# Kernel optimization log

Hardware: AMD Instinct MI355X
Metric: run time of the kernel (lower is better)

Reference implementation:

```python
import jax, jax.numpy as jnp
import numpy as np

D_MODEL = 2048
NUM_HEADS = 16
HEAD_DIM = D_MODEL // NUM_HEADS
B, T = 2, 2048


def setup_inputs() -> dict:
    key = jax.random.key(0)
    ks = jax.random.split(key, 6)
    x = jax.random.normal(ks[0], (B, T, D_MODEL), dtype=jnp.float32)
    # RoPE tables: angles theta_i = 10000^(-2i/d), half-dim tables [T, HEAD_DIM//2]
    pos = jnp.arange(T, dtype=jnp.float32)[:, None]
    inv_freq = 1.0 / (10000.0 ** (jnp.arange(0, HEAD_DIM, 2, dtype=jnp.float32) / HEAD_DIM))
    ang = pos * inv_freq[None, :]
    sin = jnp.sin(ang)
    cos = jnp.cos(ang)
    doc_ids = jnp.sort(jax.random.randint(ks[1], (B, T), 0, 4), axis=-1).astype(jnp.int32)
    W_qkv = jax.random.normal(ks[2], (D_MODEL, D_MODEL + 2 * HEAD_DIM), dtype=jnp.float32) * 0.02
    W_out = jax.random.normal(ks[3], (D_MODEL, D_MODEL), dtype=jnp.float32) * 0.02
    return {"x": x, "sin": sin, "cos": cos, "doc_ids": doc_ids, "W_qkv": W_qkv, "W_out": W_out}


def _apply_rope(x, sin, cos):
    # x: [..., T, ..., HEAD_DIM]; sin/cos: [T, HEAD_DIM//2], broadcast to x's rank
    if x.ndim == 4:  # [B, T, H, D]
        s, c = sin[None, :, None, :], cos[None, :, None, :]
    else:  # [B, T, D]
        s, c = sin[None, :, :], cos[None, :, :]
    x1, x2 = jnp.split(x, 2, axis=-1)
    return jnp.concatenate([x1 * c - x2 * s, x2 * c + x1 * s], axis=-1)


def reference(x, sin, cos, doc_ids, W_qkv, W_out):
    b, t, _ = x.shape
    qkv = x @ W_qkv  # [B, T, D_MODEL + 2*HEAD_DIM]
    q = qkv[..., :D_MODEL].reshape(b, t, NUM_HEADS, HEAD_DIM)
    k = qkv[..., D_MODEL:D_MODEL + HEAD_DIM]  # [B, T, HEAD_DIM] single KV head
    v = qkv[..., D_MODEL + HEAD_DIM:]         # [B, T, HEAD_DIM]
    q = _apply_rope(q, sin, cos)
    k = _apply_rope(k, sin, cos)
    # doc-packed causal mask -> additive bias [B, 1, T, T]
    neg_inf = jnp.finfo(q.dtype).min / 2
    causal = jnp.tril(jnp.ones((t, t), dtype=jnp.bool_))
    same_doc = doc_ids[:, :, None] == doc_ids[:, None, :]
    mask = (causal[None, :, :] & same_doc)[:, None, :, :]
    bias = jnp.where(mask, jnp.array(0.0, q.dtype), neg_inf)
    scale = 1.0 / jnp.sqrt(jnp.array(HEAD_DIM, q.dtype))
    scores = jnp.einsum("bthd,bsd->bhts", q, k) * scale + bias  # [B, H, T, T]
    attn = jax.nn.softmax(scores, axis=-1)
    out = jnp.einsum("bhts,bsd->bthd", attn, v).reshape(b, t, D_MODEL)
    return out @ W_out
```

## Files before the change

kernel.cpp:

```cpp
#include <hip/hip_runtime.h>
#include <math.h>

#define D_MODEL 2048
#define NUM_HEADS 16
#define HEAD_DIM 128
#define BB 2
#define TT 2048
#define QKV_N 2304
#define KOFF 2048
#define VOFF 2176

typedef __attribute__((ext_vector_type(8))) short short8;
typedef __attribute__((ext_vector_type(4))) float f32x4;

static __device__ __forceinline__ short f2bf(float f) {
  union { float f; unsigned u; } x; x.f = f;
  unsigned r = (x.u + 0x7FFFu + ((x.u >> 16) & 1u)) >> 16;
  return (short)r;
}
static __device__ __forceinline__ float bf2f(unsigned short u) {
  return __uint_as_float(((unsigned)u) << 16);
}

#define GLD16(gp, lp)                                              \
  __builtin_amdgcn_global_load_lds(                                \
      (const __attribute__((address_space(1))) void*)(gp),         \
      (__attribute__((address_space(3))) void*)(lp), 16, 0, 0)

static __device__ __forceinline__ void swizzle_xy(int& bx, int& by) {
  const int gx = gridDim.x;
  const int lin = blockIdx.y * gx + blockIdx.x;
  const int band = lin / (gx * 8);
  const int rem = lin - band * gx * 8;
  by = band * 8 + (rem & 7);
  bx = rem >> 3;
}

__global__ __launch_bounds__(256) void gemm_qkv_rope(
    const short* __restrict__ A, const short* __restrict__ Bt,
    short* __restrict__ qkv, short* __restrict__ Vtb,
    const float* __restrict__ sin_t, const float* __restrict__ cos_t)
{
  __shared__ short As[2 * 128 * 32];
  __shared__ short Bs[2 * 128 * 32];
  const int K = D_MODEL;

  int bx, by;
  swizzle_xy(bx, by);

  const int tid = threadIdx.x;
  const int w = tid >> 6, l = tid & 63;
  const int quad = l >> 4, l16 = l & 15;
  const int wm = w >> 1, wn = w & 1;
  const int m0 = by * 128, n0 = bx * 128;

  f32x4 acc[4][4];
#pragma unroll
  for (int i = 0; i < 4; i++)
#pragma unroll
    for (int j = 0; j < 4; j++) acc[i][j] = (f32x4){0.f, 0.f, 0.f, 0.f};

  const short* aA = A + (size_t)(m0 + w * 32 + (l >> 2)) * K + (l & 3) * 8;
  const short* aB = Bt + (size_t)(n0 + w * 32 + (l >> 2)) * K + (l & 3) * 8;
  short* lA0 = As + (w * 2) * 512;
  short* lA1 = As + (w * 2 + 1) * 512;
  short* lB0 = Bs + (w * 2) * 512;
  short* lB1 = Bs + (w * 2 + 1) * 512;

  const short* Ard = As + (size_t)(wm * 64 + l16) * 32 + quad * 8;
  const short* Brd = Bs + (size_t)(wn * 16 + l16) * 32 + quad * 8;

  for (int k0 = 0; k0 < K; k0 += 64) {
    __syncthreads();
#pragma unroll
    for (int h = 0; h < 2; h++) {
      const int go = k0 + h * 32;
      const int lo = h * 4096;
      GLD16(aA + go, lA0 + lo);
      GLD16(aA + go + (size_t)16 * K, lA1 + lo);
      GLD16(aB + go, lB0 + lo);
      GLD16(aB + go + (size_t)16 * K, lB1 + lo);
    }
    __syncthreads();

#pragma unroll
    for (int kc = 0; kc < 2; kc++) {
      short8 af[4], bf[4];
#pragma unroll
      for (int mi = 0; mi < 4; mi++)
        af[mi] = *(const short8*)(Ard + kc * 4096 + mi * 512);
#pragma unroll
      for (int ni = 0; ni < 4; ni++)
        bf[ni] = *(const short8*)(Brd + kc * 4096 + ni * 1024);
#pragma unroll
      for (int mi = 0; mi < 4; mi++)
#pragma unroll
        for (int ni = 0; ni < 4; ni++)
          acc[mi][ni] =
              __builtin_amdgcn_mfma_f32_16x16x32_bf16(af[mi], bf[ni], acc[mi][ni], 0, 0, 0);
    }
  }

  const int colbase = wn * 16 + l16;
  const bool is_v = (n0 == VOFF);

#pragma unroll
  for (int mi = 0; mi < 4; mi++) {
#pragma unroll
    for (int r = 0; r < 4; r++) {
      const int row = m0 + wm * 64 + mi * 16 + quad * 4 + r;
      const int b = row >> 11, t = row & (TT - 1);
#pragma unroll
      for (int ni = 0; ni < 2; ni++) {
        const int cloc = ni * 32 + colbase;
        const float c1 = acc[mi][ni][r];
        const float c2 = acc[mi][ni + 2][r];
        if (!is_v) {
          const float sn = sin_t[t * 64 + cloc];
          const float cs = cos_t[t * 64 + cloc];
          short* op = qkv + (size_t)row * QKV_N + n0 + cloc;
          op[0]  = f2bf(c1 * cs - c2 * sn);
          op[64] = f2bf(c2 * cs + c1 * sn);
        } else {
          Vtb[((size_t)(b * 128 + cloc) << 11) + t]      = f2bf(c1);
          Vtb[((size_t)(b * 128 + cloc + 64) << 11) + t] = f2bf(c2);
        }
      }
    }
  }
}

__global__ __launch_bounds__(256) void gemm_mfma_bt(
    const short* __restrict__ A, const short* __restrict__ Bt,
    float* __restrict__ C, int M, int N, int K)
{
  __shared__ short As[2 * 128 * 32];
  __shared__ short Bs[2 * 128 * 32];

  int bx, by;
  swizzle_xy(bx, by);

  const int tid = threadIdx.x;
  const int w = tid >> 6, l = tid & 63;
  const int quad = l >> 4, l16 = l & 15;
  const int wm = w >> 1, wn = w & 1;
  const int m0 = by * 128, n0 = bx * 128;

  f32x4 acc[4][4];
#pragma unroll
  for (int i = 0; i < 4; i++)
#pragma unroll
    for (int j = 0; j < 4; j++) acc[i][j] = (f32x4){0.f, 0.f, 0.f, 0.f};

  const short* aA = A + (size_t)(m0 + w * 32 + (l >> 2)) * K + (l & 3) * 8;
  const short* aB = Bt + (size_t)(n0 + w * 32 + (l >> 2)) * K + (l & 3) * 8;
  short* lA0 = As + (w * 2) * 512;
  short* lA1 = As + (w * 2 + 1) * 512;
  short* lB0 = Bs + (w * 2) * 512;
  short* lB1 = Bs + (w * 2 + 1) * 512;

  const short* Ard = As + (size_t)(wm * 64 + l16) * 32 + quad * 8;
  const short* Brd = Bs + (size_t)(wn * 64 + l16) * 32 + quad * 8;

  for (int k0 = 0; k0 < K; k0 += 64) {
    __syncthreads();
#pragma unroll
    for (int h = 0; h < 2; h++) {
      const int go = k0 + h * 32;
      const int lo = h * 4096;
      GLD16(aA + go, lA0 + lo);
      GLD16(aA + go + (size_t)16 * K, lA1 + lo);
      GLD16(aB + go, lB0 + lo);
      GLD16(aB + go + (size_t)16 * K, lB1 + lo);
    }
    __syncthreads();

#pragma unroll
    for (int kc = 0; kc < 2; kc++) {
      short8 af[4], bf[4];
#pragma unroll
      for (int mi = 0; mi < 4; mi++)
        af[mi] = *(const short8*)(Ard + kc * 4096 + mi * 512);
#pragma unroll
      for (int ni = 0; ni < 4; ni++)
        bf[ni] = *(const short8*)(Brd + kc * 4096 + ni * 512);
#pragma unroll
      for (int mi = 0; mi < 4; mi++)
#pragma unroll
        for (int ni = 0; ni < 4; ni++)
          acc[mi][ni] =
              __builtin_amdgcn_mfma_f32_16x16x32_bf16(af[mi], bf[ni], acc[mi][ni], 0, 0, 0);
    }
  }

#pragma unroll
  for (int mi = 0; mi < 4; mi++) {
#pragma unroll
    for (int ni = 0; ni < 4; ni++) {
#pragma unroll
      for (int r = 0; r < 4; r++) {
        const int row = m0 + wm * 64 + mi * 16 + quad * 4 + r;
        const int col = n0 + wn * 64 + ni * 16 + l16;
        C[(size_t)row * N + col] = acc[mi][ni][r];
      }
    }
  }
}

#define XB_BLOCKS 8192
#define WQ_BLOCKS (72 * 64)
#define WO_BLOCKS (64 * 64)

__global__ __launch_bounds__(256) void prep_all(
    const float* __restrict__ x, short* __restrict__ xb,
    const float* __restrict__ Wq, short* __restrict__ Wqt,
    const float* __restrict__ Wo, short* __restrict__ Wot)
{
  const int bid = blockIdx.x;
  const int tid = threadIdx.x;

  if (bid < XB_BLOCKS) {
    const size_t i4 = (size_t)bid * 256 + tid;
    float4 v = *(const float4*)(x + i4 * 4);
    short4 o;
    o.x = f2bf(v.x); o.y = f2bf(v.y); o.z = f2bf(v.z); o.w = f2bf(v.w);
    *(short4*)(xb + i4 * 4) = o;
    return;
  }

  __shared__ float t[32][33];
  const float* W;
  short* Wt;
  int N, tile, ntx;
  if (bid < XB_BLOCKS + WQ_BLOCKS) {
    tile = bid - XB_BLOCKS; W = Wq; Wt = Wqt; N = QKV_N; ntx = 72;
  } else {
    tile = bid - XB_BLOCKS - WQ_BLOCKS; W = Wo; Wt = Wot; N = D_MODEL; ntx = 64;
  }
  const int K = D_MODEL;
  const int bx = tile % ntx, byy = tile / ntx;
  const int tx = tid & 31, ty = tid >> 5;
  const int n0 = bx * 32, k0 = byy * 32;
#pragma unroll
  for (int j = 0; j < 4; j++)
    t[ty + j * 8][tx] = W[(size_t)(k0 + ty + j * 8) * N + n0 + tx];
  __syncthreads();
#pragma unroll
  for (int j = 0; j < 4; j++)
    Wt[(size_t)(n0 + ty + j * 8) * K + k0 + tx] = f2bf(t[tx][ty + j * 8]);
}

#define KSTR 136
#define VSTR 72
#define PSTR 72

__global__ __launch_bounds__(256) void attn_mfma(
    const short* __restrict__ qkv, const short* __restrict__ Vtb,
    const int* __restrict__ doc_ids, short* __restrict__ attn_out)
{
  __shared__ short Ks[64 * KSTR];
  __shared__ short Vt[128 * VSTR];
  __shared__ short Pbuf[4 * 16 * PSTR];
  __shared__ int doc_s[64];

  const int qt = blockIdx.x, h = blockIdx.y, b = blockIdx.z;
  const int q0 = qt * 64;
  const int tid = threadIdx.x;
  const int w = tid >> 6;
  const int lane = tid & 63;
  const int quad = lane >> 4, l16 = lane & 15;

  const short* qp = qkv + (size_t)(b * TT + q0 + w * 16 + l16) * QKV_N
                    + h * HEAD_DIM + quad * 8;
  short8 Qf[4];
#pragma unroll
  for (int kc = 0; kc < 4; kc++) Qf[kc] = *(const short8*)(qp + kc * 32);

  const int docmin_q = doc_ids[b * TT + q0];
  const int docmax_q = doc_ids[b * TT + q0 + 63];

  int qg[4], mydoc[4];
  float l_i[4];
#pragma unroll
  for (int r = 0; r < 4; r++) {
    qg[r] = q0 + w * 16 + quad * 4 + r;
    mydoc[r] = doc_ids[b * TT + qg[r]];
    l_i[r] = 0.f;
  }
  f32x4 O[8];
#pragma unroll
  for (int v8 = 0; v8 < 8; v8++) O[v8] = (f32x4){0.f, 0.f, 0.f, 0.f};

  short* Pw = Pbuf + w * 16 * PSTR;
  const float scale = 0.08838834764831844f;

  for (int st = 0; st <= qt; st++) {
    const int s0 = st * 64;
    const int dmin_s = doc_ids[b * TT + s0];
    const int dmax_s = doc_ids[b * TT + s0 + 63];
    if (dmax_s < docmin_q) continue;
    const bool full = (st < qt) && (dmin_s == docmax_q);

    __syncthreads();
#pragma unroll
    for (int i = 0; i < 4; i++) {
      int f = i * 256 + tid;
      int row = f >> 4, seg = f & 15;
      int4 v = *(const int4*)(qkv + (size_t)(b * TT + s0 + row) * QKV_N + KOFF + seg * 8);
      *(int4*)(Ks + row * KSTR + seg * 8) = v;
    }
#pragma unroll
    for (int i = 0; i < 4; i++) {
      int f = i * 256 + tid;
      int n = f >> 3, seg = f & 7;
      int4 v = *(const int4*)(Vtb + ((size_t)(b * 128 + n) << 11) + s0 + seg * 8);
      *(int4*)(Vt + n * VSTR + seg * 8) = v;
    }
    if (!full && tid < 64) doc_s[tid] = doc_ids[b * TT + s0 + tid];
    __syncthreads();

    f32x4 S[4];
#pragma unroll
    for (int ns = 0; ns < 4; ns++) {
      f32x4 acc = (f32x4){0.f, 0.f, 0.f, 0.f};
      const short* kr = Ks + (ns * 16 + l16) * KSTR + quad * 8;
#pragma unroll
      for (int kc = 0; kc < 4; kc++) {
        short8 kf = *(const short8*)(kr + kc * 32);
        acc = __builtin_amdgcn_mfma_f32_16x16x32_bf16(Qf[kc], kf, acc, 0, 0, 0);
      }
      S[ns] = acc;
    }

    if (full) {
#pragma unroll
      for (int ns = 0; ns < 4; ns++)
#pragma unroll
        for (int r = 0; r < 4; r++) {
          const float p = __expf(S[ns][r] * scale);
          l_i[r] += p;
          Pw[(quad * 4 + r) * PSTR + ns * 16 + l16] = f2bf(p);
        }
    } else {
#pragma unroll
      for (int ns = 0; ns < 4; ns++) {
        const int s_loc = ns * 16 + l16;
        const int sg = s0 + s_loc;
        const int sdoc = doc_s[s_loc];
#pragma unroll
        for (int r = 0; r < 4; r++) {
          const bool ok = (sg <= qg[r]) && (sdoc == mydoc[r]);
          const float p = ok ? __expf(S[ns][r] * scale) : 0.f;
          l_i[r] += p;
          Pw[(quad * 4 + r) * PSTR + ns * 16 + l16] = f2bf(p);
        }
      }
    }

#pragma unroll
    for (int ks = 0; ks < 2; ks++) {
      short8 pf = *(const short8*)(Pw + l16 * PSTR + ks * 32 + quad * 8);
#pragma unroll
      for (int v8 = 0; v8 < 8; v8++) {
        short8 vf = *(const short8*)(Vt + (v8 * 16 + l16) * VSTR + ks * 32 + quad * 8);
        O[v8] = __builtin_amdgcn_mfma_f32_16x16x32_bf16(pf, vf, O[v8], 0, 0, 0);
      }
    }
  }

#pragma unroll
  for (int off = 8; off >= 1; off >>= 1)
#pragma unroll
    for (int r = 0; r < 4; r++) l_i[r] += __shfl_xor(l_i[r], off);

#pragma unroll
  for (int r = 0; r < 4; r++) {
    const float inv = 1.f / l_i[r];
    short* op = attn_out + (size_t)(b * TT + qg[r]) * D_MODEL + h * HEAD_DIM + l16;
#pragma unroll
    for (int v8 = 0; v8 < 8; v8++)
      op[v8 * 16] = f2bf(O[v8][r] * inv);
  }
}

extern "C" void kernel_launch(void* const* d_in, const int* in_sizes, int n_in,
                              void* d_out, int out_size, void* d_ws, size_t ws_size,
                              hipStream_t stream)
{
  const float* x     = (const float*)d_in[0];
  const float* sin_t = (const float*)d_in[1];
  const float* cos_t = (const float*)d_in[2];
  const int*   doc   = (const int*)  d_in[3];
  const float* W_qkv = (const float*)d_in[4];
  const float* W_out = (const float*)d_in[5];
  float* out = (float*)d_out;

  const int M = BB * TT;

  char* p = (char*)d_ws;
  short* qkv_bf = (short*)p; p += (size_t)M * QKV_N * 2;
  short* xb     = (short*)p; p += (size_t)M * D_MODEL * 2;
  short* attn_bf = xb;
  short* Vtb    = (short*)p; p += (size_t)BB * 128 * TT * 2;
  short* Wqkv_t = (short*)p; p += (size_t)QKV_N * D_MODEL * 2;
  short* Wout_t = (short*)p;

  prep_all<<<XB_BLOCKS + WQ_BLOCKS + WO_BLOCKS, 256, 0, stream>>>(
      x, xb, W_qkv, Wqkv_t, W_out, Wout_t);

  {
    dim3 grid(QKV_N / 128, M / 128);
    gemm_qkv_rope<<<grid, 256, 0, stream>>>(xb, Wqkv_t, qkv_bf, Vtb, sin_t, cos_t);
  }
  {
    dim3 grid(TT / 64, NUM_HEADS, BB);
    attn_mfma<<<grid, 256, 0, stream>>>(qkv_bf, Vtb, doc, attn_bf);
  }
  {
    dim3 grid(D_MODEL / 128, M / 128);
    gemm_mfma_bt<<<grid, 256, 0, stream>>>(attn_bf, Wout_t, out, M, D_MODEL, D_MODEL);
  }
}
```

Baseline: 271.7 us.

## Double-buffer LDS tiles and XOR-swizzle layout in both GEMM kernels

Both GEMM kernels now use two LDS buffers, so the next K-tile is loaded with global_load_lds while MFMAs run on the current tile, and one barrier per iteration is removed. The LDS column chunks are XOR-swizzled on the global-load side and unswizzled on read, to cut LDS bank conflicts on the short8 fragment reads. This doubles LDS use per block, which may lower occupancy. Correctness depends on the swizzle being consistent between the async-load addresses and the fragment reads.

```diff
diff --git a/kernel.cpp b/kernel.cpp
--- a/kernel.cpp
+++ b/kernel.cpp
@@ -41,8 +41,8 @@
     short* __restrict__ qkv, short* __restrict__ Vtb,
     const float* __restrict__ sin_t, const float* __restrict__ cos_t)
 {
-  __shared__ short As[2 * 128 * 32];
-  __shared__ short Bs[2 * 128 * 32];
+  __shared__ short As[2][2 * 128 * 32];
+  __shared__ short Bs[2][2 * 128 * 32];
   const int K = D_MODEL;
 
   int bx, by;
@@ -60,38 +60,40 @@
 #pragma unroll
     for (int j = 0; j < 4; j++) acc[i][j] = (f32x4){0.f, 0.f, 0.f, 0.f};
 
-  const short* aA = A + (size_t)(m0 + w * 32 + (l >> 2)) * K + (l & 3) * 8;
-  const short* aB = Bt + (size_t)(n0 + w * 32 + (l >> 2)) * K + (l & 3) * 8;
-  short* lA0 = As + (w * 2) * 512;
-  short* lA1 = As + (w * 2 + 1) * 512;
-  short* lB0 = Bs + (w * 2) * 512;
-  short* lB1 = Bs + (w * 2 + 1) * 512;
-
-  const short* Ard = As + (size_t)(wm * 64 + l16) * 32 + quad * 8;
-  const short* Brd = Bs + (size_t)(wn * 16 + l16) * 32 + quad * 8;
-
-  for (int k0 = 0; k0 < K; k0 += 64) {
-    __syncthreads();
+  const int cswz = ((l & 3) ^ ((l >> 3) & 3)) * 8;
+  const short* aA = A + (size_t)(m0 + w * 32 + (l >> 2)) * K + cswz;
+  const short* aB = Bt + (size_t)(n0 + w * 32 + (l >> 2)) * K + cswz;
+  const int lwo = w * 1024;
+
+  const int aswz = (quad ^ ((l16 >> 1) & 3)) * 8;
+  const short* Ard = &As[0][0] + (size_t)(wm * 64 + l16) * 32 + aswz;
+  const short* Brd = &Bs[0][0] + (size_t)(wn * 16 + l16) * 32 + aswz;
+
+  auto stage = [&](int buf, int go0) {
 #pragma unroll
     for (int h = 0; h < 2; h++) {
-      const int go = k0 + h * 32;
-      const int lo = h * 4096;
-      GLD16(aA + go, lA0 + lo);
-      GLD16(aA + go + (size_t)16 * K, lA1 + lo);
-      GLD16(aB + go, lB0 + lo);
-      GLD16(aB + go + (size_t)16 * K, lB1 + lo);
-    }
-    __syncthreads();
-
+      const int go = go0 + h * 32;
+      short* la = &As[buf][0] + h * 4096 + lwo;
+      short* lb = &Bs[buf][0] + h * 4096 + lwo;
+      GLD16(aA + go, la);
+      GLD16(aA + go + (size_t)16 * K, la + 512);
+      GLD16(aB + go, lb);
+      GLD16(aB + go + (size_t)16 * K, lb + 512);
+    }
+  };
+
+  auto compute = [&](int buf) {
+    const short* Ac = Ard + buf * 8192;
+    const short* Bc = Brd + buf * 8192;
 #pragma unroll
     for (int kc = 0; kc < 2; kc++) {
       short8 af[4], bf[4];
 #pragma unroll
       for (int mi = 0; mi < 4; mi++)
-        af[mi] = *(const short8*)(Ard + kc * 4096 + mi * 512);
+        af[mi] = *(const short8*)(Ac + kc * 4096 + mi * 512);
 #pragma unroll
       for (int ni = 0; ni < 4; ni++)
-        bf[ni] = *(const short8*)(Brd + kc * 4096 + ni * 1024);
+        bf[ni] = *(const short8*)(Bc + kc * 4096 + ni * 1024);
 #pragma unroll
       for (int mi = 0; mi < 4; mi++)
 #pragma unroll
@@ -99,7 +101,19 @@
           acc[mi][ni] =
               __builtin_amdgcn_mfma_f32_16x16x32_bf16(af[mi], bf[ni], acc[mi][ni], 0, 0, 0);
     }
-  }
+  };
+
+  stage(0, 0);
+  __syncthreads();
+  int cur = 0;
+#pragma unroll 2
+  for (int k0 = 64; k0 < K; k0 += 64) {
+    stage(cur ^ 1, k0);
+    compute(cur);
+    __syncthreads();
+    cur ^= 1;
+  }
+  compute(cur);
 
   const int colbase = wn * 16 + l16;
   const bool is_v = (n0 == VOFF);
@@ -134,8 +148,8 @@
     const short* __restrict__ A, const short* __restrict__ Bt,
     float* __restrict__ C, int M, int N, int K)
 {
-  __shared__ short As[2 * 128 * 32];
-  __shared__ short Bs[2 * 128 * 32];
+  __shared__ short As[2][2 * 128 * 32];
+  __shared__ short Bs[2][2 * 128 * 32];
 
   int bx, by;
   swizzle_xy(bx, by);
@@ -152,38 +166,40 @@
 #pragma unroll
     for (int j = 0; j < 4; j++) acc[i][j] = (f32x4){0.f, 0.f, 0.f, 0.f};
 
-  const short* aA = A + (size_t)(m0 + w * 32 + (l >> 2)) * K + (l & 3) * 8;
-  const short* aB = Bt + (size_t)(n0 + w * 32 + (l >> 2)) * K + (l & 3) * 8;
-  short* lA0 = As + (w * 2) * 512;
-  short* lA1 = As + (w * 2 + 1) * 512;
-  short* lB0 = Bs + (w * 2) * 512;
-  short* lB1 = Bs + (w * 2 + 1) * 512;
-
-  const short* Ard = As + (size_t)(wm * 64 + l16) * 32 + quad * 8;
-  const short* Brd = Bs + (size_t)(wn * 64 + l16) * 32 + quad * 8;
-
-  for (int k0 = 0; k0 < K; k0 += 64) {
-    __syncthreads();
+  const int cswz = ((l & 3) ^ ((l >> 3) & 3)) * 8;
+  const short* aA = A + (size_t)(m0 + w * 32 + (l >> 2)) * K + cswz;
+  const short* aB = Bt + (size_t)(n0 + w * 32 + (l >> 2)) * K + cswz;
+  const int lwo = w * 1024;
+
+  const int aswz = (quad ^ ((l16 >> 1) & 3)) * 8;
+  const short* Ard = &As[0][0] + (size_t)(wm * 64 + l16) * 32 + aswz;
+  const short* Brd = &Bs[0][0] + (size_t)(wn * 64 + l16) * 32 + aswz;
+
+  auto stage = [&](int buf, int go0) {
 #pragma unroll
     for (int h = 0; h < 2; h++) {
-      const int go = k0 + h * 32;
-      const int lo = h * 4096;
-      GLD16(aA + go, lA0 + lo);
-      GLD16(aA + go + (size_t)16 * K, lA1 + lo);
-      GLD16(aB + go, lB0 + lo);
-      GLD16(aB + go + (size_t)16 * K, lB1 + lo);
-    }
-    __syncthreads();
-
+      const int go = go0 + h * 32;
+      short* la = &As[buf][0] + h * 4096 + lwo;
+      short* lb = &Bs[buf][0] + h * 4096 + lwo;
+      GLD16(aA + go, la);
+      GLD16(aA + go + (size_t)16 * K, la + 512);
+      GLD16(aB + go, lb);
+      GLD16(aB + go + (size_t)16 * K, lb + 512);
+    }
+  };
+
+  auto compute = [&](int buf) {
+    const short* Ac = Ard + buf * 8192;
+    const short* Bc = Brd + buf * 8192;
 #pragma unroll
     for (int kc = 0; kc < 2; kc++) {
       short8 af[4], bf[4];
 #pragma unroll
       for (int mi = 0; mi < 4; mi++)
-        af[mi] = *(const short8*)(Ard + kc * 4096 + mi * 512);
+        af[mi] = *(const short8*)(Ac + kc * 4096 + mi * 512);
 #pragma unroll
       for (int ni = 0; ni < 4; ni++)
-        bf[ni] = *(const short8*)(Brd + kc * 4096 + ni * 512);
+        bf[ni] = *(const short8*)(Bc + kc * 4096 + ni * 512);
 #pragma unroll
       for (int mi = 0; mi < 4; mi++)
 #pragma unroll
@@ -191,7 +207,19 @@
           acc[mi][ni] =
               __builtin_amdgcn_mfma_f32_16x16x32_bf16(af[mi], bf[ni], acc[mi][ni], 0, 0, 0);
     }
-  }
+  };
+
+  stage(0, 0);
+  __syncthreads();
+  int cur = 0;
+#pragma unroll 2
+  for (int k0 = 64; k0 < K; k0 += 64) {
+    stage(cur ^ 1, k0);
+    compute(cur);
+    __syncthreads();
+    cur ^= 1;
+  }
+  compute(cur);
 
 #pragma unroll
   for (int mi = 0; mi < 4; mi++) {
```

Measured after the change: 314.6 us. +15.8%, slower.

## Swizzle GEMM LDS tiles and register-prefetch K/V tiles in attention

Applied to the files above, without the earlier changes.

Both GEMM kernels get an XOR swizzle on the 16-byte column chunk for global-to-LDS loads and the matching MFMA fragment reads, meant to cut LDS bank conflicts. The attention kernel computes the first relevant key tile with a wave ballot instead of skipping tiles one by one. It then prefetches the next K/V tile into registers while the current tile is being computed, overlapping global loads with MFMA work. It also raises wave priority around the MFMA sections with s_setprio. The cost is more register pressure, and correctness relies on the swizzle matching between writes and reads.

```diff
diff --git a/kernel.cpp b/kernel.cpp
--- a/kernel.cpp
+++ b/kernel.cpp
@@ -60,15 +60,15 @@
 #pragma unroll
     for (int j = 0; j < 4; j++) acc[i][j] = (f32x4){0.f, 0.f, 0.f, 0.f};
 
-  const short* aA = A + (size_t)(m0 + w * 32 + (l >> 2)) * K + (l & 3) * 8;
-  const short* aB = Bt + (size_t)(n0 + w * 32 + (l >> 2)) * K + (l & 3) * 8;
-  short* lA0 = As + (w * 2) * 512;
-  short* lA1 = As + (w * 2 + 1) * 512;
-  short* lB0 = Bs + (w * 2) * 512;
-  short* lB1 = Bs + (w * 2 + 1) * 512;
-
-  const short* Ard = As + (size_t)(wm * 64 + l16) * 32 + quad * 8;
-  const short* Brd = Bs + (size_t)(wn * 16 + l16) * 32 + quad * 8;
+  const int cswz = ((l & 3) ^ ((l >> 3) & 3)) * 8;
+  const short* aA = A + (size_t)(m0 + w * 32 + (l >> 2)) * K + cswz;
+  const short* aB = Bt + (size_t)(n0 + w * 32 + (l >> 2)) * K + cswz;
+  short* lA = As + w * 1024;
+  short* lB = Bs + w * 1024;
+
+  const int aswz = (quad ^ ((l16 >> 1) & 3)) * 8;
+  const short* Ard = As + (size_t)(wm * 64 + l16) * 32 + aswz;
+  const short* Brd = Bs + (size_t)(wn * 16 + l16) * 32 + aswz;
 
   for (int k0 = 0; k0 < K; k0 += 64) {
     __syncthreads();
@@ -76,10 +76,10 @@
     for (int h = 0; h < 2; h++) {
       const int go = k0 + h * 32;
       const int lo = h * 4096;
-      GLD16(aA + go, lA0 + lo);
-      GLD16(aA + go + (size_t)16 * K, lA1 + lo);
-      GLD16(aB + go, lB0 + lo);
-      GLD16(aB + go + (size_t)16 * K, lB1 + lo);
+      GLD16(aA + go, lA + lo);
+      GLD16(aA + go + (size_t)16 * K, lA + lo + 512);
+      GLD16(aB + go, lB + lo);
+      GLD16(aB + go + (size_t)16 * K, lB + lo + 512);
     }
     __syncthreads();
 
@@ -152,15 +152,15 @@
 #pragma unroll
     for (int j = 0; j < 4; j++) acc[i][j] = (f32x4){0.f, 0.f, 0.f, 0.f};
 
-  const short* aA = A + (size_t)(m0 + w * 32 + (l >> 2)) * K + (l & 3) * 8;
-  const short* aB = Bt + (size_t)(n0 + w * 32 + (l >> 2)) * K + (l & 3) * 8;
-  short* lA0 = As + (w * 2) * 512;
-  short* lA1 = As + (w * 2 + 1) * 512;
-  short* lB0 = Bs + (w * 2) * 512;
-  short* lB1 = Bs + (w * 2 + 1) * 512;
-
-  const short* Ard = As + (size_t)(wm * 64 + l16) * 32 + quad * 8;
-  const short* Brd = Bs + (size_t)(wn * 64 + l16) * 32 + quad * 8;
+  const int cswz = ((l & 3) ^ ((l >> 3) & 3)) * 8;
+  const short* aA = A + (size_t)(m0 + w * 32 + (l >> 2)) * K + cswz;
+  const short* aB = Bt + (size_t)(n0 + w * 32 + (l >> 2)) * K + cswz;
+  short* lA = As + w * 1024;
+  short* lB = Bs + w * 1024;
+
+  const int aswz = (quad ^ ((l16 >> 1) & 3)) * 8;
+  const short* Ard = As + (size_t)(wm * 64 + l16) * 32 + aswz;
+  const short* Brd = Bs + (size_t)(wn * 64 + l16) * 32 + aswz;
 
   for (int k0 = 0; k0 < K; k0 += 64) {
     __syncthreads();
@@ -168,10 +168,10 @@
     for (int h = 0; h < 2; h++) {
       const int go = k0 + h * 32;
       const int lo = h * 4096;
-      GLD16(aA + go, lA0 + lo);
-      GLD16(aA + go + (size_t)16 * K, lA1 + lo);
-      GLD16(aB + go, lB0 + lo);
-      GLD16(aB + go + (size_t)16 * K, lB1 + lo);
+      GLD16(aA + go, lA + lo);
+      GLD16(aA + go + (size_t)16 * K, lA + lo + 512);
+      GLD16(aB + go, lB + lo);
+      GLD16(aB + go + (size_t)16 * K, lB + lo + 512);
     }
     __syncthreads();
 
@@ -262,6 +262,7 @@
   __shared__ short Vt[128 * VSTR];
   __shared__ short Pbuf[4 * 16 * PSTR];
   __shared__ int doc_s[64];
+  __shared__ int st_lo_s;
 
   const int qt = blockIdx.x, h = blockIdx.y, b = blockIdx.z;
   const int q0 = qt * 64;
@@ -279,6 +280,13 @@
   const int docmin_q = doc_ids[b * TT + q0];
   const int docmax_q = doc_ids[b * TT + q0 + 63];
 
+  if (tid < 64) {
+    const int sti = tid <= qt ? tid : qt;
+    int ok = doc_ids[b * TT + sti * 64 + 63] >= docmin_q;
+    unsigned long long m = __ballot(ok);
+    if (tid == 0) st_lo_s = (int)__ffsll(m) - 1;
+  }
+
   int qg[4], mydoc[4];
   float l_i[4];
 #pragma unroll
@@ -294,32 +302,40 @@
   short* Pw = Pbuf + w * 16 * PSTR;
   const float scale = 0.08838834764831844f;
 
-  for (int st = 0; st <= qt; st++) {
+  __syncthreads();
+  const int st_lo = st_lo_s;
+
+  int4 kreg[4], vreg[4];
+  const int kro = tid >> 4, kse = (tid & 15) * 8;
+  const int vro = tid >> 3, vse = (tid & 7) * 8;
+  auto loadKV = [&](int s0n) {
+#pragma unroll
+    for (int i = 0; i < 4; i++)
+      kreg[i] = *(const int4*)(qkv + (size_t)(b * TT + s0n + i * 16 + kro) * QKV_N + KOFF + kse);
+#pragma unroll
+    for (int i = 0; i < 4; i++)
+      vreg[i] = *(const int4*)(Vtb + ((size_t)(b * 128 + i * 32 + vro) << 11) + s0n + vse);
+  };
+
+  loadKV(st_lo * 64);
+
+  for (int st = st_lo; st <= qt; st++) {
     const int s0 = st * 64;
-    const int dmin_s = doc_ids[b * TT + s0];
-    const int dmax_s = doc_ids[b * TT + s0 + 63];
-    if (dmax_s < docmin_q) continue;
-    const bool full = (st < qt) && (dmin_s == docmax_q);
-
-    __syncthreads();
-#pragma unroll
-    for (int i = 0; i < 4; i++) {
-      int f = i * 256 + tid;
-      int row = f >> 4, seg = f & 15;
-      int4 v = *(const int4*)(qkv + (size_t)(b * TT + s0 + row) * QKV_N + KOFF + seg * 8);
-      *(int4*)(Ks + row * KSTR + seg * 8) = v;
-    }
-#pragma unroll
-    for (int i = 0; i < 4; i++) {
-      int f = i * 256 + tid;
-      int n = f >> 3, seg = f & 7;
-      int4 v = *(const int4*)(Vtb + ((size_t)(b * 128 + n) << 11) + s0 + seg * 8);
-      *(int4*)(Vt + n * VSTR + seg * 8) = v;
-    }
+    const bool full = (st < qt) && (doc_ids[b * TT + s0] == docmax_q);
+
+    __syncthreads();
+#pragma unroll
+    for (int i = 0; i < 4; i++)
+      *(int4*)(Ks + (i * 16 + kro) * KSTR + kse) = kreg[i];
+#pragma unroll
+    for (int i = 0; i < 4; i++)
+      *(int4*)(Vt + (i * 32 + vro) * VSTR + vse) = vreg[i];
     if (!full && tid < 64) doc_s[tid] = doc_ids[b * TT + s0 + tid];
+    if (st < qt) loadKV(s0 + 64);
     __syncthreads();
 
     f32x4 S[4];
+    __builtin_amdgcn_s_setprio(1);
 #pragma unroll
     for (int ns = 0; ns < 4; ns++) {
       f32x4 acc = (f32x4){0.f, 0.f, 0.f, 0.f};
@@ -331,6 +347,7 @@
       }
       S[ns] = acc;
     }
+    __builtin_amdgcn_s_setprio(0);
 
     if (full) {
 #pragma unroll
@@ -357,6 +374,7 @@
       }
     }
 
+    __builtin_amdgcn_s_setprio(1);
 #pragma unroll
     for (int ks = 0; ks < 2; ks++) {
       short8 pf = *(const short8*)(Pw + l16 * PSTR + ks * 32 + quad * 8);
@@ -366,6 +384,7 @@
         O[v8] = __builtin_amdgcn_mfma_f32_16x16x32_bf16(pf, vf, O[v8], 0, 0, 0);
       }
     }
+    __builtin_amdgcn_s_setprio(0);
   }
 
 #pragma unroll
```

New measurement: 315.3 us. 16.0% more time.
